# Kernel tuning notes

Measured on AMD Instinct MI355X. Metric: run time of the kernel, lower is better.

## Reference

```python
import jax, jax.numpy as jnp
import numpy as np

N, D_DIM, K, R = 100000, 256, 4, 16
E_RAND = 1600000
ETA, LAM, C = 0.5, 0.1, 0.5


def setup_inputs() -> dict:
    key = jax.random.key(0)
    k1, k2, k3, k4 = jax.random.split(key, 4)
    Z = jax.random.normal(k1, (N, D_DIM), jnp.float32)
    U = jax.random.normal(k2, (K, D_DIM, R), jnp.float32) / np.float32(np.sqrt(D_DIM))
    Dmat = jax.random.normal(k3, (D_DIM, D_DIM), jnp.float32) / np.float32(np.sqrt(D_DIM))
    head_w = jnp.ones((K,), jnp.float32) / K
    rnd = jax.random.randint(k4, (2, E_RAND), 0, N)
    loops = jnp.stack([jnp.arange(N), jnp.arange(N)])  # self-loops: every node has an in-edge
    edge_index = jnp.concatenate([rnd, loops], axis=1)  # [2, E]
    return {"Z": Z, "U": U, "Dmat": Dmat, "head_w": head_w, "edge_index": edge_index}


def reference(Z, U, Dmat, head_w, edge_index):
    src, dst = edge_index[0], edge_index[1]
    scale = np.float32(np.sqrt(R))

    # Project into all K subspaces at once: [K, n, r]
    ZU = jnp.einsum('nd,kdr->knr', Z, U)
    zs = ZU[:, src, :]                      # [K, E, r] gather at src
    zd = ZU[:, dst, :]                      # [K, E, r] gather at dst
    logits = (zs * zd).sum(-1) / scale      # [K, E]

    seg_max = jax.vmap(lambda l: jax.ops.segment_max(l, dst, num_segments=N))(logits)
    exp_l = jnp.exp(logits - seg_max[:, dst])
    seg_sum = jax.vmap(lambda e: jax.ops.segment_sum(e, dst, num_segments=N))(exp_l)
    alpha = exp_l / (seg_sum[:, dst] + 1e-16)  # [K, E]

    weighted = alpha[..., None] * zs           # [K, E, r]
    agg = jax.vmap(lambda w_: jax.ops.segment_sum(w_, dst, num_segments=N))(weighted)  # [K, n, r]

    w = jax.nn.softmax(head_w)
    ssa = jnp.einsum('k,knr,kdr->nd', w, agg, U)  # sum_k w_k * (agg_k @ U_k^T)

    Z_half = (1.0 - C) * Z + C * ssa

    # ISTA step (matches torch code exactly):
    DZ = Z_half @ Dmat.T
    residual = Z_half - DZ @ Dmat
    grad_step = Z_half + ETA * (residual @ Dmat)
    return jax.nn.relu(grad_step - ETA * LAM)
```

## Files before the change

### kernel.cpp

```cpp
#include <hip/hip_runtime.h>
#include <stdint.h>


typedef unsigned short u16;
typedef unsigned int u32;
typedef __attribute__((ext_vector_type(8))) short bf16x8;
typedef __attribute__((ext_vector_type(4))) float f32x4;

#define PB 256

__device__ __forceinline__ u16 f2bf(float f) {
    u32 u = __float_as_uint(f);
    u32 r = u + 0x7fffu + ((u >> 16) & 1u);
    return (u16)(r >> 16);
}

__global__ void k_prep1(const float* __restrict__ D, float* __restrict__ G) {
    int i = blockIdx.x, j = threadIdx.x;
    float acc = 0.f;
    for (int d = 0; d < 256; ++d)
        acc += D[d * 256 + i] * D[d * 256 + j];
    G[i * 256 + j] = acc;
}

__global__ void k_prep2(const float* __restrict__ D, const float* __restrict__ G,
                        float* __restrict__ A) {
    int t = blockIdx.x, j = threadIdx.x;
    float acc = 0.f;
    for (int u = 0; u < 256; ++u)
        acc += G[t * 256 + u] * D[u * 256 + j];
    A[t * 256 + j] = 0.5f * (D[t * 256 + j] - acc) + (t == j ? 1.f : 0.f);
}

__global__ void k_prep3(const float* __restrict__ A, u16* __restrict__ Bt) {
    int c = blockIdx.x, k = threadIdx.x;
    Bt[c * 320 + k] = f2bf(0.5f * A[k * 256 + c]);
}

__global__ void k_prep4(const float* __restrict__ U, const float* __restrict__ A,
                        u16* __restrict__ Bt) {
    int j = blockIdx.x, c = threadIdx.x;
    int k = j >> 4, r = j & 15;
    float acc = 0.f;
    for (int d = 0; d < 256; ++d)
        acc += U[k * 4096 + d * 16 + r] * A[d * 256 + c];
    Bt[c * 320 + 256 + j] = f2bf(0.5f * acc);
}

__global__ void k_prep5(const float* __restrict__ U, u16* __restrict__ U2t) {
    int j = blockIdx.x, d = threadIdx.x;
    U2t[j * 256 + d] = f2bf(U[(j >> 4) * 4096 + d * 16 + (j & 15)]);
}

__global__ __launch_bounds__(256) void k_cnt1(const int* __restrict__ ei,
                                              int* __restrict__ cnt2, int E, int nbuck) {
    __shared__ int h[512];
    int t = threadIdx.x, b = blockIdx.x;
    for (int i = t; i < nbuck; i += 256) h[i] = 0;
    __syncthreads();
    int per = (E + PB - 1) / PB;
    int lo = b * per;
    int hi = lo + per; if (hi > E) hi = E;
    for (int e = lo + t; e < hi; e += 256)
        atomicAdd(&h[ei[E + e] >> 8], 1);
    __syncthreads();
    for (int i = t; i < nbuck; i += 256)
        cnt2[b * nbuck + i] = h[i];
}

__global__ __launch_bounds__(256) void k_cscan1(const int* __restrict__ cnt2,
                                                int* __restrict__ pre2,
                                                int* __restrict__ tot, int nbuck) {
    __shared__ int s[256];
    int t = threadIdx.x, b = blockIdx.x;
    int v = cnt2[t * nbuck + b];
    s[t] = v;
    __syncthreads();
    for (int o = 1; o < 256; o <<= 1) {
        int x = (t >= o) ? s[t - o] : 0;
        __syncthreads();
        s[t] += x;
        __syncthreads();
    }
    pre2[t * nbuck + b] = s[t] - v;
    if (t == 255) tot[b] = s[255];
}

__global__ __launch_bounds__(512) void k_cscan2(const int* __restrict__ tot,
                                                int* __restrict__ bbase, int nbuck) {
    __shared__ int s[512];
    int t = threadIdx.x;
    int v = (t < nbuck) ? tot[t] : 0;
    s[t] = v;
    __syncthreads();
    for (int o = 1; o < 512; o <<= 1) {
        int x = (t >= o) ? s[t - o] : 0;
        __syncthreads();
        s[t] += x;
        __syncthreads();
    }
    if (t < nbuck) bbase[t] = s[t] - v;
}

__global__ __launch_bounds__(256) void k_place(const int* __restrict__ ei,
                                               const int* __restrict__ pre2,
                                               const int* __restrict__ bbase,
                                               int* __restrict__ part, int E, int nbuck) {
    __shared__ int baseS[512];
    __shared__ int cur[512];
    int t = threadIdx.x, b = blockIdx.x;
    for (int i = t; i < nbuck; i += 256) {
        baseS[i] = bbase[i] + pre2[b * nbuck + i];
        cur[i] = 0;
    }
    __syncthreads();
    int per = (E + PB - 1) / PB;
    int lo = b * per;
    int hi = lo + per; if (hi > E) hi = E;
    for (int e = lo + t; e < hi; e += 256) {
        int s = ei[e];
        int d = ei[E + e];
        int bk = d >> 8;
        int r = atomicAdd(&cur[bk], 1);
        part[baseS[bk] + r] = (s << 8) | (d & 255);
    }
}

__global__ __launch_bounds__(256) void k_bucket(const int* __restrict__ part,
                                                const int* __restrict__ tot,
                                                const int* __restrict__ bbase,
                                                int* __restrict__ off,
                                                int* __restrict__ cnt,
                                                int* __restrict__ esrc, int n) {
    __shared__ int ncnt[256], excl[256], cur[256], sc[256];
    int t = threadIdx.x, b = blockIdx.x;
    ncnt[t] = 0;
    cur[t] = 0;
    __syncthreads();
    int base = bbase[b], m = tot[b];
    for (int i = t; i < m; i += 256)
        atomicAdd(&ncnt[part[base + i] & 255], 1);
    __syncthreads();
    int v = ncnt[t];
    sc[t] = v;
    __syncthreads();
    for (int o = 1; o < 256; o <<= 1) {
        int x = (t >= o) ? sc[t - o] : 0;
        __syncthreads();
        sc[t] += x;
        __syncthreads();
    }
    excl[t] = sc[t] - v;
    int node = b * 256 + t;
    if (node < n) {
        off[node] = base + excl[t];
        cnt[node] = v;
    }
    __syncthreads();
    for (int i = t; i < m; i += 256) {
        int pk = part[base + i];
        int j = pk & 255;
        int r = atomicAdd(&cur[j], 1);
        esrc[base + excl[j] + r] = pk >> 8;
    }
}

__global__ __launch_bounds__(256) void k_cast(const float* __restrict__ Z,
                                              u16* __restrict__ Zb, int total8) {
    int i = blockIdx.x * 256 + threadIdx.x;
    if (i >= total8) return;
    const float4* zp = reinterpret_cast<const float4*>(Z + (size_t)i * 8);
    float4 a = zp[0], b = zp[1];
    uint4 pk;
    pk.x = (u32)f2bf(a.x) | ((u32)f2bf(a.y) << 16);
    pk.y = (u32)f2bf(a.z) | ((u32)f2bf(a.w) << 16);
    pk.z = (u32)f2bf(b.x) | ((u32)f2bf(b.y) << 16);
    pk.w = (u32)f2bf(b.z) | ((u32)f2bf(b.w) << 16);
    *reinterpret_cast<uint4*>(Zb + (size_t)i * 8) = pk;
}

__global__ __launch_bounds__(256) void k_zumm(const u16* __restrict__ Zb,
                                              const u16* __restrict__ U2t,
                                              float* __restrict__ ZU, int n) {
    const int t = threadIdx.x;
    const int w = t >> 6;
    const int lane = t & 63;
    const int m16 = lane & 15;
    const int quad = lane >> 4;
    const int nb = blockIdx.x * 64 + w * 16;

    int row = nb + m16;
    int rowc = row < n ? row : n - 1;

    f32x4 acc[4];
#pragma unroll
    for (int nt = 0; nt < 4; ++nt) acc[nt] = (f32x4){0.f, 0.f, 0.f, 0.f};

    for (int ks = 0; ks < 8; ++ks) {
        bf16x8 a = *reinterpret_cast<const bf16x8*>(
            Zb + (size_t)rowc * 256 + ks * 32 + quad * 8);
#pragma unroll
        for (int nt = 0; nt < 4; ++nt) {
            bf16x8 b = *reinterpret_cast<const bf16x8*>(
                U2t + (size_t)(nt * 16 + m16) * 256 + ks * 32 + quad * 8);
            acc[nt] = __builtin_amdgcn_mfma_f32_16x16x32_bf16(a, b, acc[nt], 0, 0, 0);
        }
    }
#pragma unroll
    for (int r = 0; r < 4; ++r) {
        int node = nb + quad * 4 + r;
        if (node < n) {
#pragma unroll
            for (int nt = 0; nt < 4; ++nt)
                ZU[(size_t)node * 64 + nt * 16 + m16] = acc[nt][r];
        }
    }
}

__global__ __launch_bounds__(256) void k_agg(const float* __restrict__ ZU,
                                             const int* __restrict__ esrc,
                                             const int* __restrict__ off,
                                             const int* __restrict__ cnt,
                                             const float* __restrict__ hwp,
                                             u16* __restrict__ Vb, int n) {
    int node = blockIdx.x * 4 + (threadIdx.x >> 6);
    int lane = threadIdx.x & 63;
    if (node >= n) return;
    const int q = lane & 15;
    const int g = lane >> 4;
    float4 zd4 = *reinterpret_cast<const float4*>(&ZU[(size_t)node * 64 + q * 4]);
    int base = off[node];
    int deg = cnt[node];

    float ax = 0.f, ay = 0.f, az = 0.f, aw = 0.f, ssum = 0.f;
    for (int c0 = 0; c0 < deg; c0 += 4) {
        int e = c0 + g;
        bool valid = e < deg;
        int s = valid ? esrc[base + e] : 0;
        float4 zs4 = *reinterpret_cast<const float4*>(&ZU[(size_t)s * 64 + q * 4]);
        float p = zs4.x * zd4.x + zs4.y * zd4.y + zs4.z * zd4.z + zs4.w * zd4.w;
        p += __shfl_xor(p, 1);
        p += __shfl_xor(p, 2);
        float ew = valid ? __expf(p * 0.25f) : 0.f;
        ax += ew * zs4.x; ay += ew * zs4.y;
        az += ew * zs4.z; aw += ew * zs4.w;
        ssum += ew;
    }
    ax += __shfl_xor(ax, 16); ax += __shfl_xor(ax, 32);
    ay += __shfl_xor(ay, 16); ay += __shfl_xor(ay, 32);
    az += __shfl_xor(az, 16); az += __shfl_xor(az, 32);
    aw += __shfl_xor(aw, 16); aw += __shfl_xor(aw, 32);
    ssum += __shfl_xor(ssum, 16); ssum += __shfl_xor(ssum, 32);

    if (g == 0) {
        float h0 = hwp[0], h1 = hwp[1], h2 = hwp[2], h3 = hwp[3];
        float mx = fmaxf(fmaxf(h0, h1), fmaxf(h2, h3));
        float e0 = __expf(h0 - mx), e1 = __expf(h1 - mx),
              e2 = __expf(h2 - mx), e3 = __expf(h3 - mx);
        float es = e0 + e1 + e2 + e3;
        int hd = q >> 2;
        float wk = (hd == 0 ? e0 : hd == 1 ? e1 : hd == 2 ? e2 : e3) / es;
        float inv = wk / ssum;
        uint2 pk;
        pk.x = (u32)f2bf(ax * inv) | ((u32)f2bf(ay * inv) << 16);
        pk.y = (u32)f2bf(az * inv) | ((u32)f2bf(aw * inv) << 16);
        *reinterpret_cast<uint2*>(&Vb[(size_t)node * 64 + q * 4]) = pk;
    }
}

__global__ __launch_bounds__(256) void k_out(const u16* __restrict__ Zb,
                                             const u16* __restrict__ Vb,
                                             const u16* __restrict__ Bt,
                                             float* __restrict__ out, int n) {
    const int t = threadIdx.x;
    const int w = t >> 6;
    const int lane = t & 63;
    const int m16 = lane & 15;
    const int quad = lane >> 4;
    const int nb = blockIdx.x * 64;

    f32x4 acc[4][4];
#pragma unroll
    for (int mt = 0; mt < 4; ++mt)
#pragma unroll
        for (int nt = 0; nt < 4; ++nt)
            acc[mt][nt] = (f32x4){0.f, 0.f, 0.f, 0.f};

    int rowc[4];
#pragma unroll
    for (int mt = 0; mt < 4; ++mt) {
        int r = nb + mt * 16 + m16;
        rowc[mt] = r < n ? r : n - 1;
    }
    const u16* bbase4[4];
#pragma unroll
    for (int nt = 0; nt < 4; ++nt)
        bbase4[nt] = Bt + (size_t)(w * 64 + nt * 16 + m16) * 320 + quad * 8;

    for (int ks = 0; ks < 8; ++ks) {
        bf16x8 a[4], b[4];
#pragma unroll
        for (int mt = 0; mt < 4; ++mt)
            a[mt] = *reinterpret_cast<const bf16x8*>(
                Zb + (size_t)rowc[mt] * 256 + ks * 32 + quad * 8);
#pragma unroll
        for (int nt = 0; nt < 4; ++nt)
            b[nt] = *reinterpret_cast<const bf16x8*>(bbase4[nt] + ks * 32);
#pragma unroll
        for (int mt = 0; mt < 4; ++mt)
#pragma unroll
            for (int nt = 0; nt < 4; ++nt)
                acc[mt][nt] = __builtin_amdgcn_mfma_f32_16x16x32_bf16(
                    a[mt], b[nt], acc[mt][nt], 0, 0, 0);
    }
#pragma unroll
    for (int ks = 8; ks < 10; ++ks) {
        bf16x8 a[4], b[4];
#pragma unroll
        for (int mt = 0; mt < 4; ++mt)
            a[mt] = *reinterpret_cast<const bf16x8*>(
                Vb + (size_t)rowc[mt] * 64 + (ks - 8) * 32 + quad * 8);
#pragma unroll
        for (int nt = 0; nt < 4; ++nt)
            b[nt] = *reinterpret_cast<const bf16x8*>(bbase4[nt] + ks * 32);
#pragma unroll
        for (int mt = 0; mt < 4; ++mt)
#pragma unroll
            for (int nt = 0; nt < 4; ++nt)
                acc[mt][nt] = __builtin_amdgcn_mfma_f32_16x16x32_bf16(
                    a[mt], b[nt], acc[mt][nt], 0, 0, 0);
    }

#pragma unroll
    for (int mt = 0; mt < 4; ++mt) {
#pragma unroll
        for (int r = 0; r < 4; ++r) {
            int row = nb + mt * 16 + quad * 4 + r;
            if (row < n) {
#pragma unroll
                for (int nt = 0; nt < 4; ++nt) {
                    int col = w * 64 + nt * 16 + m16;
                    out[(size_t)row * 256 + col] =
                        fmaxf(acc[mt][nt][r] - 0.05f, 0.f);
                }
            }
        }
    }
}

extern "C" void kernel_launch(void* const* d_in, const int* in_sizes, int n_in,
                              void* d_out, int out_size, void* d_ws, size_t ws_size,
                              hipStream_t stream) {
    const float* Z  = (const float*)d_in[0];
    const float* U  = (const float*)d_in[1];
    const float* Dm = (const float*)d_in[2];
    const float* hw = (const float*)d_in[3];
    const int*   ei = (const int*)d_in[4];
    const int n = in_sizes[0] / 256;
    const int E = in_sizes[4] / 2;
    float* out = (float*)d_out;
    const int nbuck = (n + 255) >> 8;

    char* wp = (char*)d_ws;
    float* ZUb  = (float*)wp;
    u16* Zb     = (u16*)(wp + (size_t)n * 256);
    int* part   = (int*)Zb;
    int* cnt2   = part + E;
    int* pre2   = cnt2 + PB * nbuck;
    u16* Vb     = Zb + (size_t)n * 256;
    float* G    = (float*)(Vb + (size_t)n * 64);
    float* A    = G + 65536;
    u16* Bt     = (u16*)(A + 65536);
    u16* U2t    = Bt + 256 * 320;
    int* esrc   = (int*)(U2t + 64 * 256);
    int* off    = esrc + E;
    int* cnt    = off + n;
    int* tot    = cnt + n;
    int* bbase  = tot + nbuck;

    k_prep1<<<256, 256, 0, stream>>>(Dm, G);
    k_prep2<<<256, 256, 0, stream>>>(Dm, G, A);
    k_prep3<<<256, 256, 0, stream>>>(A, Bt);
    k_prep4<<<64, 256, 0, stream>>>(U, A, Bt);
    k_prep5<<<64, 256, 0, stream>>>(U, U2t);

    k_cnt1<<<PB, 256, 0, stream>>>(ei, cnt2, E, nbuck);
    k_cscan1<<<nbuck, 256, 0, stream>>>(cnt2, pre2, tot, nbuck);
    k_cscan2<<<1, 512, 0, stream>>>(tot, bbase, nbuck);
    k_place<<<PB, 256, 0, stream>>>(ei, pre2, bbase, part, E, nbuck);
    k_bucket<<<nbuck, 256, 0, stream>>>(part, tot, bbase, off, cnt, esrc, n);

    k_cast<<<(n * 256 / 8 + 255) / 256, 256, 0, stream>>>(Z, Zb, n * 32);
    k_zumm<<<(n + 63) / 64, 256, 0, stream>>>(Zb, U2t, ZUb, n);
    k_agg<<<(n + 3) / 4, 256, 0, stream>>>(ZUb, esrc, off, cnt, hw, Vb, n);
    k_out<<<(n + 63) / 64, 256, 0, stream>>>(Zb, Vb, Bt, out, n);
}
```

Before: 470.2 us.

## Fuse Z cast into projection GEMM and stage A tiles in swizzled LDS

Removes the separate fp32-to-bf16 cast kernel. The projection kernel now reads Z, converts it, writes the bf16 copy for later use, and keeps the 64-row tile in XOR-swizzled shared memory for its MFMA loads. The output GEMM likewise stages its Zb and Vb row tiles in swizzled LDS, so the four waves no longer each re-read the same A rows from global memory. The cost is a block-wide barrier, 32-40 KB of LDS per block that may reduce occupancy, and extra store traffic from the fused kernel.

Result: faster. 444.8 us (-5.4%).

```diff
diff --git a/kernel.cpp b/kernel.cpp
--- a/kernel.cpp
+++ b/kernel.cpp
@@ -165,40 +165,48 @@
     }
 }
 
-__global__ __launch_bounds__(256) void k_cast(const float* __restrict__ Z,
-                                              u16* __restrict__ Zb, int total8) {
-    int i = blockIdx.x * 256 + threadIdx.x;
-    if (i >= total8) return;
-    const float4* zp = reinterpret_cast<const float4*>(Z + (size_t)i * 8);
-    float4 a = zp[0], b = zp[1];
-    uint4 pk;
-    pk.x = (u32)f2bf(a.x) | ((u32)f2bf(a.y) << 16);
-    pk.y = (u32)f2bf(a.z) | ((u32)f2bf(a.w) << 16);
-    pk.z = (u32)f2bf(b.x) | ((u32)f2bf(b.y) << 16);
-    pk.w = (u32)f2bf(b.z) | ((u32)f2bf(b.w) << 16);
-    *reinterpret_cast<uint4*>(Zb + (size_t)i * 8) = pk;
-}
-
-__global__ __launch_bounds__(256) void k_zumm(const u16* __restrict__ Zb,
+__global__ __launch_bounds__(256) void k_zumm(const float* __restrict__ Z,
                                               const u16* __restrict__ U2t,
-                                              float* __restrict__ ZU, int n) {
+                                              float* __restrict__ ZU,
+                                              u16* __restrict__ Zb, int n) {
+    __shared__ __align__(16) u16 sA[64 * 256];
     const int t = threadIdx.x;
     const int w = t >> 6;
     const int lane = t & 63;
     const int m16 = lane & 15;
     const int quad = lane >> 4;
-    const int nb = blockIdx.x * 64 + w * 16;
-
-    int row = nb + m16;
-    int rowc = row < n ? row : n - 1;
+    const int nb = blockIdx.x * 64;
+
+#pragma unroll
+    for (int i = 0; i < 8; ++i) {
+        int c = i * 256 + t;
+        int row = c >> 5, col = c & 31;
+        int grow = nb + row;
+        int gr = grow < n ? grow : n - 1;
+        const float4* zp = reinterpret_cast<const float4*>(Z + (size_t)gr * 256 + col * 8);
+        float4 a = zp[0], b = zp[1];
+        uint4 pk;
+        pk.x = (u32)f2bf(a.x) | ((u32)f2bf(a.y) << 16);
+        pk.y = (u32)f2bf(a.z) | ((u32)f2bf(a.w) << 16);
+        pk.z = (u32)f2bf(b.x) | ((u32)f2bf(b.y) << 16);
+        pk.w = (u32)f2bf(b.z) | ((u32)f2bf(b.w) << 16);
+        *reinterpret_cast<uint4*>((char*)sA + row * 512 + ((col ^ (row & 7)) << 4)) = pk;
+        if (grow < n)
+            *reinterpret_cast<uint4*>(Zb + (size_t)grow * 256 + col * 8) = pk;
+    }
+    __syncthreads();
 
     f32x4 acc[4];
 #pragma unroll
     for (int nt = 0; nt < 4; ++nt) acc[nt] = (f32x4){0.f, 0.f, 0.f, 0.f};
+
+    const int arow = w * 16 + m16;
+    const u32 abase = (u32)arow * 512;
+    const u32 asw = (u32)(m16 & 7) << 4;
 
     for (int ks = 0; ks < 8; ++ks) {
         bf16x8 a = *reinterpret_cast<const bf16x8*>(
-            Zb + (size_t)rowc * 256 + ks * 32 + quad * 8);
+            (char*)sA + abase + (((u32)(ks * 64 + quad * 16)) ^ asw));
 #pragma unroll
         for (int nt = 0; nt < 4; ++nt) {
             bf16x8 b = *reinterpret_cast<const bf16x8*>(
@@ -208,7 +216,7 @@
     }
 #pragma unroll
     for (int r = 0; r < 4; ++r) {
-        int node = nb + quad * 4 + r;
+        int node = nb + w * 16 + quad * 4 + r;
         if (node < n) {
 #pragma unroll
             for (int nt = 0; nt < 4; ++nt)
@@ -272,6 +280,8 @@
                                              const u16* __restrict__ Vb,
                                              const u16* __restrict__ Bt,
                                              float* __restrict__ out, int n) {
+    __shared__ __align__(16) u16 sA[64 * 256];
+    __shared__ __align__(16) u16 sV[64 * 64];
     const int t = threadIdx.x;
     const int w = t >> 6;
     const int lane = t & 63;
@@ -279,6 +289,24 @@
     const int quad = lane >> 4;
     const int nb = blockIdx.x * 64;
 
+#pragma unroll
+    for (int i = 0; i < 8; ++i) {
+        int c = i * 256 + t;
+        int row = c >> 5, col = c & 31;
+        int gr = nb + row; if (gr >= n) gr = n - 1;
+        uint4 pk = *reinterpret_cast<const uint4*>(Zb + (size_t)gr * 256 + col * 8);
+        *reinterpret_cast<uint4*>((char*)sA + row * 512 + ((col ^ (row & 7)) << 4)) = pk;
+    }
+#pragma unroll
+    for (int i = 0; i < 2; ++i) {
+        int c = i * 256 + t;
+        int row = c >> 3, col = c & 7;
+        int gr = nb + row; if (gr >= n) gr = n - 1;
+        uint4 pk = *reinterpret_cast<const uint4*>(Vb + (size_t)gr * 64 + col * 8);
+        *reinterpret_cast<uint4*>((char*)sV + row * 128 + ((col ^ (row & 7)) << 4)) = pk;
+    }
+    __syncthreads();
+
     f32x4 acc[4][4];
 #pragma unroll
     for (int mt = 0; mt < 4; ++mt)
@@ -286,23 +314,20 @@
         for (int nt = 0; nt < 4; ++nt)
             acc[mt][nt] = (f32x4){0.f, 0.f, 0.f, 0.f};
 
-    int rowc[4];
-#pragma unroll
-    for (int mt = 0; mt < 4; ++mt) {
-        int r = nb + mt * 16 + m16;
-        rowc[mt] = r < n ? r : n - 1;
-    }
     const u16* bbase4[4];
 #pragma unroll
     for (int nt = 0; nt < 4; ++nt)
         bbase4[nt] = Bt + (size_t)(w * 64 + nt * 16 + m16) * 320 + quad * 8;
 
+    const u32 asw = (u32)(m16 & 7) << 4;
+
     for (int ks = 0; ks < 8; ++ks) {
         bf16x8 a[4], b[4];
 #pragma unroll
         for (int mt = 0; mt < 4; ++mt)
             a[mt] = *reinterpret_cast<const bf16x8*>(
-                Zb + (size_t)rowc[mt] * 256 + ks * 32 + quad * 8);
+                (char*)sA + (u32)(mt * 16 + m16) * 512 +
+                (((u32)(ks * 64 + quad * 16)) ^ asw));
 #pragma unroll
         for (int nt = 0; nt < 4; ++nt)
             b[nt] = *reinterpret_cast<const bf16x8*>(bbase4[nt] + ks * 32);
@@ -319,7 +344,8 @@
 #pragma unroll
         for (int mt = 0; mt < 4; ++mt)
             a[mt] = *reinterpret_cast<const bf16x8*>(
-                Vb + (size_t)rowc[mt] * 64 + (ks - 8) * 32 + quad * 8);
+                (char*)sV + (u32)(mt * 16 + m16) * 128 +
+                (((u32)((ks - 8) * 64 + quad * 16)) ^ asw));
 #pragma unroll
         for (int nt = 0; nt < 4; ++nt)
             b[nt] = *reinterpret_cast<const bf16x8*>(bbase4[nt] + ks * 32);
@@ -390,8 +416,7 @@
     k_place<<<PB, 256, 0, stream>>>(ei, pre2, bbase, part, E, nbuck);
     k_bucket<<<nbuck, 256, 0, stream>>>(part, tot, bbase, off, cnt, esrc, n);
 
-    k_cast<<<(n * 256 / 8 + 255) / 256, 256, 0, stream>>>(Z, Zb, n * 32);
-    k_zumm<<<(n + 63) / 64, 256, 0, stream>>>(Zb, U2t, ZUb, n);
+    k_zumm<<<(n + 63) / 64, 256, 0, stream>>>(Z, U2t, ZUb, Zb, n);
     k_agg<<<(n + 3) / 4, 256, 0, stream>>>(ZUb, esrc, off, cnt, hw, Vb, n);
     k_out<<<(n + 63) / 64, 256, 0, stream>>>(Zb, Vb, Bt, out, n);
 }
```
